# Kernel tuning notes

Hardware: AMD Instinct MI355X
Metric: run time of the kernel (lower is better)

Reference implementation:

```python
import jax, jax.numpy as jnp
import numpy as np

B, F, D = 8192, 1024, 128  # batch, agent input feats, latent (Bernoulli) size


def setup_inputs() -> dict:
    key = jax.random.key(0)
    kx, kw = jax.random.split(key)
    x = jax.random.normal(kx, (B, F), dtype=jnp.float32)
    # scale so logits land in a non-degenerate range around [0,1]
    W = jax.random.normal(kw, (F, D), dtype=jnp.float32) * (1.0 / np.sqrt(F))
    b = jnp.zeros((D,), dtype=jnp.float32)
    return {"x": x, "W": W, "b": b}


def reference(x, W, b):
    """SparseMAPWrapper.forward with a linear agent, budget=0 (bernoulli_smap).

    SparseMAP over independent Bernoullis: mu* = clip(theta, 0, 1); the sparse
    distribution over bit-vector configurations is the nested-threshold
    decomposition of mu* (support <= D+1), padded with zero-weight rows.
    """
    theta = x @ W + b                      # [B, D] logits from the agent
    mu = jnp.clip(theta, 0.0, 1.0)         # SparseMAP marginals
    u = -jnp.sort(-mu, axis=-1)            # [B, D] descending
    # configs c_j = 1[mu >= u_j]; prepend the all-zeros configuration
    configs = (mu[:, None, :] >= u[:, :, None]).astype(theta.dtype)  # [B, D, D]
    zero_cfg = jnp.zeros((mu.shape[0], 1, mu.shape[1]), dtype=theta.dtype)
    sample = jnp.concatenate([zero_cfg, configs], axis=1)            # [B, D+1, D]
    # weights: w0 = 1 - u_1 (all-zeros), w_j = u_j - u_{j+1}, u_{D+1} = 0
    u_next = jnp.concatenate([u[:, 1:], jnp.zeros_like(u[:, :1])], axis=1)
    distr = jnp.concatenate([1.0 - u[:, :1], u - u_next], axis=1)    # [B, D+1]
    pos = distr > 0
    safe = jnp.where(pos, distr, 1.0)
    entropy_distr = jnp.sum(jnp.where(pos, -distr * jnp.log(safe), 0.0))
    entropy_distr = entropy_distr / distr.shape[0]
    support = jnp.sum(pos, axis=-1)        # [B] per-sample support sizes
    return sample, distr, entropy_distr, support
```

## Files before the change

kernel.cpp:

```cpp
#include <hip/hip_runtime.h>
#include <hip/hip_bf16.h>
#include <math.h>

#define BATCH 8192
#define FEAT  1024
#define DLAT  128
#define DP1   129

typedef float f32x4 __attribute__((ext_vector_type(4)));

#define TILE_M 32
#define KT     32
#define NK0    (FEAT / KT)

__global__ __launch_bounds__(256) void gemm_theta(
    const float* __restrict__ x, const float* __restrict__ W,
    const float* __restrict__ b, float* __restrict__ theta) {
  __shared__ __align__(16) float xs[2][TILE_M][KT];
  __shared__ __align__(16) float wsh[2][KT][DLAT];
  const int row0 = blockIdx.x * TILE_M;
  const int t = threadIdx.x;
  const int c4 = (t & 31) * 4;
  const int r4 = (t >> 5) * 4;

  const int lxr = t >> 3;
  const int lxc = (t & 7) * 4;
  float acc[4][4] = {{0.f}};

  {
    float4 px = *(const float4*)(x + (size_t)(row0 + lxr) * FEAT + lxc);
    *(float4*)&xs[0][lxr][lxc] = px;
    #pragma unroll
    for (int i = 0; i < 4; ++i) {
      const int idx = t + i * 256;
      const int kk  = idx >> 5;
      const int cq  = (idx & 31) * 4;
      *(float4*)&wsh[0][kk][cq] = *(const float4*)(W + (size_t)kk * DLAT + cq);
    }
  }
  __syncthreads();

  int buf = 0;
  for (int k0it = 0; k0it < NK0; ++k0it) {
    float4 px;
    float4 pw[4];
    const bool hasNext = (k0it + 1 < NK0);
    if (hasNext) {
      const int k0n = (k0it + 1) * KT;
      px = *(const float4*)(x + (size_t)(row0 + lxr) * FEAT + k0n + lxc);
      #pragma unroll
      for (int i = 0; i < 4; ++i) {
        const int idx = t + i * 256;
        const int kk  = idx >> 5;
        const int cq  = (idx & 31) * 4;
        pw[i] = *(const float4*)(W + (size_t)(k0n + kk) * DLAT + cq);
      }
    }

    #pragma unroll
    for (int kk = 0; kk < KT; kk += 4) {
      float4 xv[4], wv[4];
      #pragma unroll
      for (int r = 0; r < 4; ++r) xv[r] = *(const float4*)&xs[buf][r4 + r][kk];
      #pragma unroll
      for (int i = 0; i < 4; ++i) wv[i] = *(const float4*)&wsh[buf][kk + i][c4];
      #pragma unroll
      for (int r = 0; r < 4; ++r) {
        const float* xr = (const float*)&xv[r];
        #pragma unroll
        for (int i = 0; i < 4; ++i) {
          const float* wc = (const float*)&wv[i];
          #pragma unroll
          for (int c = 0; c < 4; ++c)
            acc[r][c] = fmaf(xr[i], wc[c], acc[r][c]);
        }
      }
    }

    if (hasNext) {
      *(float4*)&xs[buf ^ 1][lxr][lxc] = px;
      #pragma unroll
      for (int i = 0; i < 4; ++i) {
        const int idx = t + i * 256;
        const int kk  = idx >> 5;
        const int cq  = (idx & 31) * 4;
        *(float4*)&wsh[buf ^ 1][kk][cq] = pw[i];
      }
    }
    __syncthreads();
    buf ^= 1;
  }

  const float4 bv = *(const float4*)(b + c4);
  #pragma unroll
  for (int r = 0; r < 4; ++r) {
    float4 o;
    o.x = acc[r][0] + bv.x;
    o.y = acc[r][1] + bv.y;
    o.z = acc[r][2] + bv.z;
    o.w = acc[r][3] + bv.w;
    *(float4*)(theta + (size_t)(row0 + r4 + r) * DLAT + c4) = o;
  }
}

__global__ __launch_bounds__(256) void smap_rows(
    const float* __restrict__ theta, float* __restrict__ sample,
    float* __restrict__ distr, float* __restrict__ support,
    float* __restrict__ entpart) {
  __shared__ __align__(16) float mu[DLAT];
  __shared__ __align__(16) float s[DLAT];
  __shared__ float red[256];
  __shared__ int   redi[256];
  const int row = blockIdx.x;
  const int t = threadIdx.x;

  if (t < DLAT) {
    float v = theta[(size_t)row * DLAT + t];
    v = fminf(fmaxf(v, 0.0f), 1.0f);
    mu[t] = v;
  }
  __syncthreads();

  if (t < DLAT) {
    const float v = mu[t];
    int rank = 0;
    #pragma unroll
    for (int q = 0; q < DLAT / 4; ++q) {
      const float4 m4 = *(const float4*)&mu[q * 4];
      rank += (m4.x > v || (m4.x == v && (q * 4 + 0) < t)) ? 1 : 0;
      rank += (m4.y > v || (m4.y == v && (q * 4 + 1) < t)) ? 1 : 0;
      rank += (m4.z > v || (m4.z == v && (q * 4 + 2) < t)) ? 1 : 0;
      rank += (m4.w > v || (m4.w == v && (q * 4 + 3) < t)) ? 1 : 0;
    }
    s[rank] = v;
  }
  __syncthreads();

  float w = 0.0f; int pos = 0; float ent = 0.0f;
  if (t < DP1) {
    if (t == 0)          w = 1.0f - s[0];
    else if (t < DLAT)   w = s[t - 1] - s[t];
    else                 w = s[DLAT - 1];
    distr[(size_t)row * DP1 + t] = w;
    if (w > 0.0f) { pos = 1; ent = -w * logf(w); }
  }
  red[t] = ent; redi[t] = pos;
  __syncthreads();
  for (int off = 128; off > 0; off >>= 1) {
    if (t < off) { red[t] += red[t + off]; redi[t] += redi[t + off]; }
    __syncthreads();
  }
  if (t == 0) {
    entpart[row] = red[0];
    support[row] = (float)redi[0];
  }

  const int jl = t >> 5;
  const int cq = (t & 31) * 4;
  f32x4* out = (f32x4*)(sample + (size_t)row * DP1 * DLAT);
  const float4 m4 = *(const float4*)&mu[cq];
  #pragma unroll
  for (int it = 0; it < 16; ++it) {
    const int j = it * 8 + jl;
    const float thr = (j == 0) ? 2.0f : s[j - 1];
    f32x4 o;
    o.x = (m4.x >= thr) ? 1.0f : 0.0f;
    o.y = (m4.y >= thr) ? 1.0f : 0.0f;
    o.z = (m4.z >= thr) ? 1.0f : 0.0f;
    o.w = (m4.w >= thr) ? 1.0f : 0.0f;
    __builtin_nontemporal_store(o, &out[(size_t)j * (DLAT / 4) + (cq >> 2)]);
  }
  if (jl == 0) {
    const float thr = s[DLAT - 1];
    f32x4 o;
    o.x = (m4.x >= thr) ? 1.0f : 0.0f;
    o.y = (m4.y >= thr) ? 1.0f : 0.0f;
    o.z = (m4.z >= thr) ? 1.0f : 0.0f;
    o.w = (m4.w >= thr) ? 1.0f : 0.0f;
    __builtin_nontemporal_store(o, &out[(size_t)DLAT * (DLAT / 4) + (cq >> 2)]);
  }
}

__global__ __launch_bounds__(1024) void reduce_ent(
    const float* __restrict__ entpart, float* __restrict__ outent) {
  __shared__ double red[1024];
  const int t = threadIdx.x;
  double acc = 0.0;
  for (int i = t; i < BATCH; i += 1024) acc += (double)entpart[i];
  red[t] = acc;
  __syncthreads();
  for (int off = 512; off > 0; off >>= 1) {
    if (t < off) red[t] += red[t + off];
    __syncthreads();
  }
  if (t == 0) *outent = (float)(red[0] / (double)BATCH);
}

extern "C" void kernel_launch(void* const* d_in, const int* in_sizes, int n_in,
                              void* d_out, int out_size, void* d_ws, size_t ws_size,
                              hipStream_t stream) {
  const float* x = (const float*)d_in[0];
  const float* W = (const float*)d_in[1];
  const float* b = (const float*)d_in[2];

  float* out = (float*)d_out;
  const size_t n_sample = (size_t)BATCH * DP1 * DLAT;
  const size_t n_distr  = (size_t)BATCH * DP1;
  float* sample  = out;
  float* distr   = out + n_sample;
  float* entropy = out + n_sample + n_distr;
  float* support = out + n_sample + n_distr + 1;

  float* theta   = (float*)d_ws;
  float* entpart = theta + (size_t)BATCH * DLAT;

  gemm_theta<<<BATCH / TILE_M, 256, 0, stream>>>(x, W, b, theta);
  smap_rows<<<BATCH, 256, 0, stream>>>(theta, sample, distr, support, entpart);
  reduce_ent<<<1, 1024, 0, stream>>>(entpart, entropy);
}
```

Before: 622.3 us.

## Halve GEMM row tile, use wave-shuffle reductions, issue sample stores first

The GEMM tile drops from 32 to 16 rows per block, doubling the block count to 512 so more CUs stay busy, at the cost of fewer FMAs per W load. In the per-row SMAP kernel, the shared-memory tree reduction with nine barriers is replaced by 64-lane wave shuffles plus one barrier. The large sample stores are moved ahead of the reduction so they are issued earlier, and distr is written with nontemporal stores. The kernel is dominated by the roughly 540 MB sample write, so these changes mostly trim latency around it.

Result: slower. 644.7 us (+3.6%).

```diff
diff --git a/kernel.cpp b/kernel.cpp
--- a/kernel.cpp
+++ b/kernel.cpp
@@ -9,7 +9,7 @@
 
 typedef float f32x4 __attribute__((ext_vector_type(4)));
 
-#define TILE_M 32
+#define TILE_M 16
 #define KT     32
 #define NK0    (FEAT / KT)
 
@@ -21,15 +21,16 @@
   const int row0 = blockIdx.x * TILE_M;
   const int t = threadIdx.x;
   const int c4 = (t & 31) * 4;
-  const int r4 = (t >> 5) * 4;
+  const int r2 = (t >> 5) * 2;
 
   const int lxr = t >> 3;
   const int lxc = (t & 7) * 4;
-  float acc[4][4] = {{0.f}};
+  float acc[2][4] = {{0.f}};
 
   {
-    float4 px = *(const float4*)(x + (size_t)(row0 + lxr) * FEAT + lxc);
-    *(float4*)&xs[0][lxr][lxc] = px;
+    if (t < 128)
+      *(float4*)&xs[0][lxr][lxc] =
+          *(const float4*)(x + (size_t)(row0 + lxr) * FEAT + lxc);
     #pragma unroll
     for (int i = 0; i < 4; ++i) {
       const int idx = t + i * 256;
@@ -47,7 +48,8 @@
     const bool hasNext = (k0it + 1 < NK0);
     if (hasNext) {
       const int k0n = (k0it + 1) * KT;
-      px = *(const float4*)(x + (size_t)(row0 + lxr) * FEAT + k0n + lxc);
+      if (t < 128)
+        px = *(const float4*)(x + (size_t)(row0 + lxr) * FEAT + k0n + lxc);
       #pragma unroll
       for (int i = 0; i < 4; ++i) {
         const int idx = t + i * 256;
@@ -59,13 +61,13 @@
 
     #pragma unroll
     for (int kk = 0; kk < KT; kk += 4) {
-      float4 xv[4], wv[4];
-      #pragma unroll
-      for (int r = 0; r < 4; ++r) xv[r] = *(const float4*)&xs[buf][r4 + r][kk];
+      float4 xv[2], wv[4];
+      #pragma unroll
+      for (int r = 0; r < 2; ++r) xv[r] = *(const float4*)&xs[buf][r2 + r][kk];
       #pragma unroll
       for (int i = 0; i < 4; ++i) wv[i] = *(const float4*)&wsh[buf][kk + i][c4];
       #pragma unroll
-      for (int r = 0; r < 4; ++r) {
+      for (int r = 0; r < 2; ++r) {
         const float* xr = (const float*)&xv[r];
         #pragma unroll
         for (int i = 0; i < 4; ++i) {
@@ -78,7 +80,7 @@
     }
 
     if (hasNext) {
-      *(float4*)&xs[buf ^ 1][lxr][lxc] = px;
+      if (t < 128) *(float4*)&xs[buf ^ 1][lxr][lxc] = px;
       #pragma unroll
       for (int i = 0; i < 4; ++i) {
         const int idx = t + i * 256;
@@ -93,13 +95,13 @@
 
   const float4 bv = *(const float4*)(b + c4);
   #pragma unroll
-  for (int r = 0; r < 4; ++r) {
+  for (int r = 0; r < 2; ++r) {
     float4 o;
     o.x = acc[r][0] + bv.x;
     o.y = acc[r][1] + bv.y;
     o.z = acc[r][2] + bv.z;
     o.w = acc[r][3] + bv.w;
-    *(float4*)(theta + (size_t)(row0 + r4 + r) * DLAT + c4) = o;
+    *(float4*)(theta + (size_t)(row0 + r2 + r) * DLAT + c4) = o;
   }
 }
 
@@ -109,8 +111,8 @@
     float* __restrict__ entpart) {
   __shared__ __align__(16) float mu[DLAT];
   __shared__ __align__(16) float s[DLAT];
-  __shared__ float red[256];
-  __shared__ int   redi[256];
+  __shared__ float entw[4];
+  __shared__ int   posw[4];
   const int row = blockIdx.x;
   const int t = threadIdx.x;
 
@@ -136,48 +138,51 @@
   }
   __syncthreads();
 
+  {
+    const int jl = t >> 5;
+    const int cq = (t & 31) * 4;
+    f32x4* out = (f32x4*)(sample + (size_t)row * DP1 * DLAT);
+    const float4 m4 = *(const float4*)&mu[cq];
+    #pragma unroll
+    for (int it = 0; it < 16; ++it) {
+      const int j = it * 8 + jl;
+      const float thr = (j == 0) ? 2.0f : s[j - 1];
+      f32x4 o;
+      o.x = (m4.x >= thr) ? 1.0f : 0.0f;
+      o.y = (m4.y >= thr) ? 1.0f : 0.0f;
+      o.z = (m4.z >= thr) ? 1.0f : 0.0f;
+      o.w = (m4.w >= thr) ? 1.0f : 0.0f;
+      __builtin_nontemporal_store(o, &out[(size_t)j * (DLAT / 4) + (cq >> 2)]);
+    }
+    if (jl == 0) {
+      const float thr = s[DLAT - 1];
+      f32x4 o;
+      o.x = (m4.x >= thr) ? 1.0f : 0.0f;
+      o.y = (m4.y >= thr) ? 1.0f : 0.0f;
+      o.z = (m4.z >= thr) ? 1.0f : 0.0f;
+      o.w = (m4.w >= thr) ? 1.0f : 0.0f;
+      __builtin_nontemporal_store(o, &out[(size_t)DLAT * (DLAT / 4) + (cq >> 2)]);
+    }
+  }
+
   float w = 0.0f; int pos = 0; float ent = 0.0f;
   if (t < DP1) {
     if (t == 0)          w = 1.0f - s[0];
     else if (t < DLAT)   w = s[t - 1] - s[t];
     else                 w = s[DLAT - 1];
-    distr[(size_t)row * DP1 + t] = w;
+    __builtin_nontemporal_store(w, &distr[(size_t)row * DP1 + t]);
     if (w > 0.0f) { pos = 1; ent = -w * logf(w); }
   }
-  red[t] = ent; redi[t] = pos;
-  __syncthreads();
-  for (int off = 128; off > 0; off >>= 1) {
-    if (t < off) { red[t] += red[t + off]; redi[t] += redi[t + off]; }
-    __syncthreads();
-  }
+  #pragma unroll
+  for (int off = 32; off > 0; off >>= 1) {
+    ent += __shfl_xor(ent, off, 64);
+    pos += __shfl_xor(pos, off, 64);
+  }
+  if ((t & 63) == 0) { entw[t >> 6] = ent; posw[t >> 6] = pos; }
+  __syncthreads();
   if (t == 0) {
-    entpart[row] = red[0];
-    support[row] = (float)redi[0];
-  }
-
-  const int jl = t >> 5;
-  const int cq = (t & 31) * 4;
-  f32x4* out = (f32x4*)(sample + (size_t)row * DP1 * DLAT);
-  const float4 m4 = *(const float4*)&mu[cq];
-  #pragma unroll
-  for (int it = 0; it < 16; ++it) {
-    const int j = it * 8 + jl;
-    const float thr = (j == 0) ? 2.0f : s[j - 1];
-    f32x4 o;
-    o.x = (m4.x >= thr) ? 1.0f : 0.0f;
-    o.y = (m4.y >= thr) ? 1.0f : 0.0f;
-    o.z = (m4.z >= thr) ? 1.0f : 0.0f;
-    o.w = (m4.w >= thr) ? 1.0f : 0.0f;
-    __builtin_nontemporal_store(o, &out[(size_t)j * (DLAT / 4) + (cq >> 2)]);
-  }
-  if (jl == 0) {
-    const float thr = s[DLAT - 1];
-    f32x4 o;
-    o.x = (m4.x >= thr) ? 1.0f : 0.0f;
-    o.y = (m4.y >= thr) ? 1.0f : 0.0f;
-    o.z = (m4.z >= thr) ? 1.0f : 0.0f;
-    o.w = (m4.w >= thr) ? 1.0f : 0.0f;
-    __builtin_nontemporal_store(o, &out[(size_t)DLAT * (DLAT / 4) + (cq >> 2)]);
+    entpart[row] = (entw[0] + entw[1]) + (entw[2] + entw[3]);
+    support[row] = (float)(posw[0] + posw[1] + posw[2] + posw[3]);
   }
 }
 
```
